# Kernel tuning notes

Measured on AMD Instinct MI355X. Metric: run time of the kernel, lower is better.

## Reference

```python
import jax, jax.numpy as jnp
import numpy as np

EPS = 1e-5
NUM_HEADS = 12
HEAD_DIM = 64


def _split_heads(x, H, hd):
    B, S, _ = x.shape
    return x.reshape(B, S, H, hd).transpose(0, 2, 1, 3)  # [B,H,S,hd]


def _rope_rotate(x, pos, freqs):
    # x: [B,H,S,hd]; pos: [B,S,nd] int; freqs: [nd,H,hd//2]
    ang = jnp.einsum('bsd,dhf->bhsf', pos.astype(x.dtype), freqs)  # [B,H,S,hd//2]
    cos, sin = jnp.cos(ang), jnp.sin(ang)
    B, H, S, hd = x.shape
    xp = x.reshape(B, H, S, hd // 2, 2)
    xr, xi = xp[..., 0], xp[..., 1]
    out = jnp.stack([xr * cos - xi * sin, xr * sin + xi * cos], axis=-1)
    return out.reshape(B, H, S, hd)


def setup_inputs() -> dict:
    key = jax.random.key(0)
    ks = jax.random.split(key, 8)
    B, Sq, Sk, D = 4, 1024, 1024, 768
    return {
        'q': jax.random.normal(ks[0], (B, Sq, D), jnp.float32),
        'kv': jax.random.normal(ks[1], (B, Sk, D), jnp.float32),
        'posq': jax.random.randint(ks[2], (B, Sq, 2), 0, 32, jnp.int32),
        'posk': jax.random.randint(ks[3], (B, Sk, 2), 0, 32, jnp.int32),
        'w_norm': jnp.ones((D,), jnp.float32),
        'w_q': jax.random.normal(ks[4], (D, D), jnp.float32) * 0.02,
        'b_q': jnp.zeros((D,), jnp.float32),
        'w_kv': jax.random.normal(ks[5], (2 * D, D), jnp.float32) * 0.02,
        'b_kv': jnp.zeros((2 * D,), jnp.float32),
        'w_out': jax.random.normal(ks[6], (D, D), jnp.float32) * 0.02,
        'b_out': jnp.zeros((D,), jnp.float32),
        'freqs': jax.random.normal(ks[7], (2, NUM_HEADS, HEAD_DIM // 2), jnp.float32),
    }


def reference(q, kv, posq, posk, w_norm, w_q, b_q, w_kv, b_kv, w_out, b_out, freqs):
    B, Sq, D = q.shape
    H, hd = NUM_HEADS, HEAD_DIM
    # RMSNorm on q
    qn = q * jax.lax.rsqrt(jnp.mean(q * q, axis=-1, keepdims=True) + EPS) * w_norm
    # projections (torch F.linear: x @ W.T + b)
    qp = qn @ w_q.T + b_q
    kvp = kv @ w_kv.T + b_kv
    k, v = jnp.split(kvp, 2, axis=-1)
    qh = _split_heads(qp, H, hd)
    kh = _split_heads(k, H, hd)
    vh = _split_heads(v, H, hd)
    # ND mixed RoPE
    qh = _rope_rotate(qh, posq, freqs)
    kh = _rope_rotate(kh, posk, freqs)
    # SDPA
    scale = 1.0 / np.sqrt(hd)
    scores = jnp.einsum('bhqd,bhkd->bhqk', qh, kh) * scale
    attn = jax.nn.softmax(scores, axis=-1)
    o = jnp.einsum('bhqk,bhkd->bhqd', attn, vh)
    o = o.transpose(0, 2, 1, 3).reshape(B, Sq, H * hd)
    return o @ w_out.T + b_out
```

## Files before the change

kernel.cpp:

```cpp
#include <hip/hip_runtime.h>

#define B_   4
#define S_   1024
#define D_   768
#define H_   12
#define HD_  64
#define NROW (B_*S_)
#define RSTRIDE (H_*HD_)
#define NBH  (B_*H_)
#define LOG2E 1.44269504f

typedef __bf16 bf16_t;
typedef bf16_t bf16x8 __attribute__((ext_vector_type(8)));
typedef float  f32x4  __attribute__((ext_vector_type(4)));
typedef float  f32x16 __attribute__((ext_vector_type(16)));
typedef unsigned int u32x4 __attribute__((ext_vector_type(4)));

__device__ __forceinline__ unsigned short bf16b(float f){
  bf16_t b = (bf16_t)f;
  return __builtin_bit_cast(unsigned short, b);
}

__device__ __forceinline__ void gload16(const void* g, void* l){
  __builtin_amdgcn_global_load_lds(
      (const __attribute__((address_space(1))) void*)g,
      (__attribute__((address_space(3))) void*)l, 16, 0, 0);
}

__device__ __forceinline__ unsigned int cvtpk(float lo, float hi){
  unsigned int r;
  asm("v_cvt_pk_bf16_f32 %0, %1, %2" : "=v"(r) : "v"(lo), "v"(hi));
  return r;
}

__device__ __forceinline__ void plswap(unsigned int &a, unsigned int &b){
  asm volatile("v_permlane32_swap_b32 %0, %1" : "+v"(a), "+v"(b));
}

__global__ void prep_kernel(const float* __restrict__ q, const float* __restrict__ w_norm,
                            bf16_t* __restrict__ qn,
                            const float* __restrict__ wq,  bf16_t* __restrict__ wqb,
                            const float* __restrict__ wkv, bf16_t* __restrict__ wkvb,
                            const float* __restrict__ wo,  bf16_t* __restrict__ wob,
                            const float* __restrict__ kv,  bf16_t* __restrict__ kvb){
  int bid = blockIdx.x;
  if (bid < NROW){
    int row = bid;
    const float* src = q + (size_t)row*D_;
    float vals[3]; float ss = 0.f;
#pragma unroll
    for (int i=0;i<3;i++){ float v = src[threadIdx.x + i*256]; vals[i]=v; ss += v*v; }
#pragma unroll
    for (int m=1;m<64;m<<=1) ss += __shfl_xor(ss, m, 64);
    __shared__ float red[4];
    if ((threadIdx.x & 63) == 0) red[threadIdx.x>>6] = ss;
    __syncthreads();
    float tot = red[0]+red[1]+red[2]+red[3];
    float rs = rsqrtf(tot*(1.0f/D_) + 1e-5f);
#pragma unroll
    for (int i=0;i<3;i++){
      int c = threadIdx.x + i*256;
      qn[(size_t)row*D_ + c] = (bf16_t)(vals[i]*rs*w_norm[c]);
    }
  } else {
    int i = (bid - NROW)*256 + threadIdx.x;
    const int n0 = D_*D_/4, n1 = 2*D_*D_/4, n2 = D_*D_/4, n3 = NROW*D_/4;
    const float* s; bf16_t* d; int off;
    if (i < n0){ s = wq; d = wqb; off = i; }
    else if (i < n0+n1){ s = wkv; d = wkvb; off = i - n0; }
    else if (i < n0+n1+n2){ s = wo; d = wob; off = i - n0 - n1; }
    else if (i < n0+n1+n2+n3){ s = kv; d = kvb; off = i - n0 - n1 - n2; }
    else return;
    float4 v = reinterpret_cast<const float4*>(s)[off];
    ushort4 o;
    o.x = bf16b(v.x); o.y = bf16b(v.y); o.z = bf16b(v.z); o.w = bf16b(v.w);
    reinterpret_cast<ushort4*>(d)[off] = o;
  }
}

template<int TM, int TN>
__device__ __forceinline__ void gemm_core_t(const bf16_t* __restrict__ A, const bf16_t* __restrict__ W,
                                            int K, int row0, int col0,
                                            bf16_t* As, bf16_t* Bs,
                                            f32x4 (&acc)[TM/32][TN/32]){
  const int tid  = threadIdx.x;
  const int lane = tid & 63;
  const int wv   = tid >> 6;
  const int wr = wv >> 1, wc = wv & 1;
  const int l4 = lane >> 4, lm = lane & 15;

  for (int kt = 0; kt < K; kt += 64){
#pragma unroll
    for (int i=0;i<TM/32;i++){
      int c = i*256 + tid;
      int r = c >> 3, kc = (c & 7) ^ (r & 7);
      gload16(A + (size_t)(row0+r)*K + kt + kc*8, As + (size_t)(i*256 + wv*64)*8);
    }
#pragma unroll
    for (int i=0;i<TN/32;i++){
      int c = i*256 + tid;
      int r = c >> 3, kc = (c & 7) ^ (r & 7);
      gload16(W + (size_t)(col0+r)*K + kt + kc*8, Bs + (size_t)(i*256 + wv*64)*8);
    }
    __syncthreads();

#pragma unroll
    for (int kk=0; kk<2; kk++){
      bf16x8 af[TM/32], bfr[TN/32];
#pragma unroll
      for (int mi=0;mi<TM/32;mi++){
        int r = wr*(TM/2) + mi*16 + lm;
        int s = (kk*4 + l4) ^ (r & 7);
        af[mi] = *reinterpret_cast<const bf16x8*>(As + r*64 + s*8);
      }
#pragma unroll
      for (int ni=0;ni<TN/32;ni++){
        int r = wc*(TN/2) + ni*16 + lm;
        int s = (kk*4 + l4) ^ (r & 7);
        bfr[ni] = *reinterpret_cast<const bf16x8*>(Bs + r*64 + s*8);
      }
#pragma unroll
      for (int mi=0;mi<TM/32;mi++)
#pragma unroll
        for (int ni=0;ni<TN/32;ni++)
          acc[mi][ni] = __builtin_amdgcn_mfma_f32_16x16x32_bf16(af[mi], bfr[ni], acc[mi][ni], 0,0,0);
    }
    __syncthreads();
  }
}

__global__ void gemm_kernel(const bf16_t* __restrict__ A, const bf16_t* __restrict__ W,
                            const float* __restrict__ bias, float* __restrict__ C,
                            int N, int K){
  __shared__ bf16_t As[64*64];
  __shared__ bf16_t Bs[64*64];
  int l = ((int)blockIdx.x & 7)*96 + ((int)blockIdx.x >> 3);
  int x = l & 63, y = l >> 6;
  f32x4 acc[2][2] = {};
  gemm_core_t<64,64>(A, W, K, x*64, y*64, As, Bs, acc);
  const int lane = threadIdx.x & 63;
  const int wv   = threadIdx.x >> 6;
  const int wr = wv >> 1, wc = wv & 1;
  const int l4 = lane >> 4, lm = lane & 15;
  const int row0 = x*64, col0 = y*64;
#pragma unroll
  for (int mi=0;mi<2;mi++){
#pragma unroll
    for (int ni=0;ni<2;ni++){
      int col = col0 + wc*32 + ni*16 + lm;
      float bv = bias[col];
#pragma unroll
      for (int j=0;j<4;j++){
        int row = row0 + wr*32 + mi*16 + l4*4 + j;
        C[(size_t)row*N + col] = acc[mi][ni][j] + bv;
      }
    }
  }
}

__device__ __forceinline__ void epi_rope(f32x4 (&acc)[2][4], const float* __restrict__ bias,
                                         const int* __restrict__ pos, const float* __restrict__ freqs,
                                         bf16_t* __restrict__ dst, int row0, int col0, float scale){
  const int lane = threadIdx.x & 63;
  const int wv   = threadIdx.x >> 6;
  const int wr = wv >> 1, wc = wv & 1;
  const int l4 = lane >> 4, lm = lane & 15;
  const int par = lm & 1;
#pragma unroll
  for (int ni=0;ni<4;ni++){
    int col = col0 + wc*64 + ni*16 + lm;
    int h = col >> 6, hd = col & 63, f = hd >> 1;
    float F1 = freqs[h*32 + f];
    float F2 = freqs[H_*32 + h*32 + f];
    float bv = bias[col];
    int cc = f >> 3, hi = (f >> 2) & 1;
    int ebase = cc*512 + hi*256 + (f&3)*2 + par;
#pragma unroll
    for (int mi=0;mi<2;mi++){
#pragma unroll
      for (int j=0;j<4;j++){
        int row = row0 + wr*32 + mi*16 + l4*4 + j;
        float v = acc[mi][ni][j] + bv;
        float vp = __shfl_xor(v, 1, 64);
        float p0 = (float)pos[row*2+0], p1 = (float)pos[row*2+1];
        float ang = p0*F1 + p1*F2;
        float sn, cs;
        __sincosf(ang, &sn, &cs);
        float out = (par ? (vp*sn + v*cs) : (v*cs - vp*sn)) * scale;
        int b = row >> 10, s = row & 1023;
        int bh = b*H_ + h, tile = s >> 5, lq = s & 31;
        dst[((size_t)(bh*32 + tile))*2048 + ebase + lq*8] = (bf16_t)out;
      }
    }
  }
}

__device__ __forceinline__ void epi_vpack(f32x4 (&acc)[2][4], const float* __restrict__ bias,
                                          bf16_t* __restrict__ vfrag, int row0, int col0){
  const int lane = threadIdx.x & 63;
  const int wv   = threadIdx.x >> 6;
  const int wr = wv >> 1, wc = wv & 1;
  const int l4 = lane >> 4, lm = lane & 15;
#pragma unroll
  for (int ni=0;ni<4;ni++){
    int col = col0 + wc*64 + ni*16 + lm;
    int vcol = col - D_;
    int h = vcol >> 6, d = vcol & 63;
    int dt = d >> 5, lq2 = d & 31;
    float bv = bias[col];
    int ebase = dt*1024 + lq2*8;
#pragma unroll
    for (int mi=0;mi<2;mi++){
#pragma unroll
      for (int j=0;j<4;j++){
        int row = row0 + wr*32 + mi*16 + l4*4 + j;
        int b = row >> 10, s = row & 1023;
        int bh = b*H_ + h;
        int kb = s >> 5, ks = (s >> 4) & 1, hi2 = (s >> 3) & 1, jj = s & 7;
        vfrag[((size_t)(bh*32 + kb))*2048 + ebase + ks*512 + hi2*256 + jj]
            = (bf16_t)(acc[mi][ni][j] + bv);
      }
    }
  }
}

__global__ void gemm_qkv_kernel(const bf16_t* __restrict__ qn, const bf16_t* __restrict__ kvb,
                                const bf16_t* __restrict__ wq, const bf16_t* __restrict__ wkv,
                                const float* __restrict__ bq, const float* __restrict__ bkv,
                                const int* __restrict__ posq, const int* __restrict__ posk,
                                const float* __restrict__ freqs,
                                bf16_t* __restrict__ qh, bf16_t* __restrict__ kh,
                                bf16_t* __restrict__ vfrag){
  __shared__ bf16_t As[64*64];
  __shared__ bf16_t Bs[128*64];
  int l = ((int)blockIdx.x & 7)*144 + ((int)blockIdx.x >> 3);
  int x = l & 63, y = l >> 6;
  f32x4 acc[2][4] = {};
  if (y < 6){
    gemm_core_t<64,128>(qn, wq, D_, x*64, y*128, As, Bs, acc);
    epi_rope(acc, bq, posq, freqs, qh, x*64, y*128, 0.125f*LOG2E);
  } else {
    int c0 = (y-6)*128;
    gemm_core_t<64,128>(kvb, wkv, D_, x*64, c0, As, Bs, acc);
    if (y < 12)
      epi_rope(acc, bkv, posk, freqs, kh, x*64, c0, 1.0f);
    else
      epi_vpack(acc, bkv, vfrag, x*64, c0);
  }
}

__device__ __forceinline__ void attn_step(const bf16x8 (&kf)[4], const bf16x8 (&vf)[4],
                                          const bf16x8 (&qf)[4], f32x16 (&acc_o)[2],
                                          float &psum){
  f32x16 accs = {};
#pragma unroll
  for (int c=0;c<4;c++)
    accs = __builtin_amdgcn_mfma_f32_32x32x16_bf16(kf[c], qf[c], accs, 0,0,0);
#pragma unroll
  for (int r=0;r<16;r++){
    float v = exp2f(accs[r]);
    accs[r] = v;
    psum += v;
  }
  bf16x8 pa[2];
#pragma unroll
  for (int ks=0;ks<2;ks++){
    const int base = ks*8;
    unsigned int a0 = cvtpk(accs[base+0], accs[base+1]);
    unsigned int a1 = cvtpk(accs[base+2], accs[base+3]);
    unsigned int b0 = cvtpk(accs[base+4], accs[base+5]);
    unsigned int b1 = cvtpk(accs[base+6], accs[base+7]);
    plswap(a0, b0);
    plswap(a1, b1);
    u32x4 w; w[0]=a0; w[1]=a1; w[2]=b0; w[3]=b1;
    pa[ks] = __builtin_bit_cast(bf16x8, w);
  }
#pragma unroll
  for (int dt=0;dt<2;dt++)
#pragma unroll
    for (int ks=0;ks<2;ks++)
      acc_o[dt] = __builtin_amdgcn_mfma_f32_32x32x16_bf16(pa[ks], vf[dt*2+ks], acc_o[dt], 0,0,0);
}

__global__ __launch_bounds__(256, 3)
void attn_kernel(const bf16_t* __restrict__ Qf, const bf16_t* __restrict__ Kf,
                 const bf16_t* __restrict__ Vf, bf16_t* __restrict__ Oh){
  const int lane = threadIdx.x & 63;
  const int wv   = threadIdx.x >> 6;
  const int hi = lane >> 5, lq = lane & 31;
  int l = ((int)blockIdx.x & 7)*192 + ((int)blockIdx.x >> 3);
  const int bh = l >> 5;
  const int qt = l & 31;
  const int q0 = qt*32;
  const int b = bh / H_, h = bh % H_;
  const size_t headoff = ((size_t)b*S_*H_ + h)*HD_;

  __shared__ float part[4][64][33];
  __shared__ float ps[4][32];

  bf16x8 qf[4];
  {
    const bf16_t* qp_ = Qf + (size_t)(bh*32 + qt)*2048 + lane*8;
#pragma unroll
    for (int c=0;c<4;c++)
      qf[c] = *reinterpret_cast<const bf16x8*>(qp_ + c*512);
  }

  const bf16_t* kbase = Kf + ((size_t)bh*32 + wv*8)*2048 + lane*8;
  const bf16_t* vbase = Vf + ((size_t)bh*32 + wv*8)*2048 + lane*8;

  float psum = 0.f;
  f32x16 acc_o[2] = {};

  bf16x8 kfA[4], kfB[4], vf[4];
#pragma unroll
  for (int c=0;c<4;c++)
    kfA[c] = *reinterpret_cast<const bf16x8*>(kbase + c*512);

#pragma unroll
  for (int t=0; t<4; ++t){
    {
      const bf16_t* vp = vbase + (size_t)(2*t)*2048;
#pragma unroll
      for (int j=0;j<4;j++) vf[j] = *reinterpret_cast<const bf16x8*>(vp + j*512);
      const bf16_t* kp = kbase + (size_t)(2*t+1)*2048;
#pragma unroll
      for (int c=0;c<4;c++) kfB[c] = *reinterpret_cast<const bf16x8*>(kp + c*512);
      attn_step(kfA, vf, qf, acc_o, psum);
    }
    {
      const bf16_t* vp = vbase + (size_t)(2*t+1)*2048;
#pragma unroll
      for (int j=0;j<4;j++) vf[j] = *reinterpret_cast<const bf16x8*>(vp + j*512);
      if (t < 3){
        const bf16_t* kp = kbase + (size_t)(2*t+2)*2048;
#pragma unroll
        for (int c=0;c<4;c++) kfA[c] = *reinterpret_cast<const bf16x8*>(kp + c*512);
      }
      attn_step(kfB, vf, qf, acc_o, psum);
    }
  }

  float tp = psum + __shfl_xor(psum, 32, 64);
#pragma unroll
  for (int dt=0;dt<2;dt++)
#pragma unroll
    for (int r=0;r<16;r++)
      part[wv][lane][dt*16+r] = acc_o[dt][r];
  if (lane < 32) ps[wv][lq] = tp;
  __syncthreads();

  const int dt = wv >> 1;
  const int rbase = (wv & 1)*8;
  float tot = ps[0][lq] + ps[1][lq] + ps[2][lq] + ps[3][lq];
  float inv = 1.0f / tot;

  bf16_t* obase = Oh + headoff;
#pragma unroll
  for (int ri=0;ri<8;ri++){
    int r = rbase + ri;
    float s = part[0][lane][dt*16+r] + part[1][lane][dt*16+r]
            + part[2][lane][dt*16+r] + part[3][lane][dt*16+r];
    float invr = __shfl(inv, (r&3) + 8*(r>>2) + 4*hi, 64);
    int qq = q0 + (r&3) + 8*(r>>2) + 4*hi;
    obase[(size_t)qq*RSTRIDE + dt*32 + lq] = (bf16_t)(s*invr);
  }
}

extern "C" void kernel_launch(void* const* d_in, const int* in_sizes, int n_in,
                              void* d_out, int out_size, void* d_ws, size_t ws_size,
                              hipStream_t stream) {
  const float* q      = (const float*)d_in[0];
  const float* kv     = (const float*)d_in[1];
  const int*   posq   = (const int*)d_in[2];
  const int*   posk   = (const int*)d_in[3];
  const float* w_norm = (const float*)d_in[4];
  const float* w_q    = (const float*)d_in[5];
  const float* b_q    = (const float*)d_in[6];
  const float* w_kv   = (const float*)d_in[7];
  const float* b_kv   = (const float*)d_in[8];
  const float* w_out  = (const float*)d_in[9];
  const float* b_out  = (const float*)d_in[10];
  const float* freqs  = (const float*)d_in[11];
  float* out = (float*)d_out;

  char* p = (char*)d_ws;
  bf16_t* qn   = (bf16_t*)p; p += (size_t)NROW*D_*2;
  bf16_t* kvb  = (bf16_t*)p; p += (size_t)NROW*D_*2;
  bf16_t* wqb  = (bf16_t*)p; p += (size_t)D_*D_*2;
  bf16_t* wkvb = (bf16_t*)p; p += (size_t)2*D_*D_*2;
  bf16_t* wob  = (bf16_t*)p; p += (size_t)D_*D_*2;
  bf16_t* qh   = (bf16_t*)p; p += (size_t)NROW*D_*2;
  bf16_t* kh   = (bf16_t*)p; p += (size_t)NROW*D_*2;
  bf16_t* vt   = (bf16_t*)p; p += (size_t)NBH*HD_*S_*2;
  bf16_t* oh   = (bf16_t*)p; p += (size_t)NROW*D_*2;

  prep_kernel<<<NROW + 5376, 256, 0, stream>>>(q, w_norm, qn,
                                               w_q, wqb, w_kv, wkvb, w_out, wob, kv, kvb);
  gemm_qkv_kernel<<<1152, 256, 0, stream>>>(qn, kvb, wqb, wkvb, b_q, b_kv,
                                            posq, posk, freqs, qh, kh, vt);
  attn_kernel<<<1536, 256, 0, stream>>>(qh, kh, vt, oh);
  gemm_kernel<<<768, 256, 0, stream>>>(oh, wob, b_out, out, D_, D_);
}
```

Baseline: 76.31 us.

## Double-buffer LDS tiles in GEMM cores to overlap loads with MFMA

Splits the GEMM core into separate stage and compute helpers and adds a ping-pong pair of LDS buffers. The next K-tile's global-to-LDS loads are issued before the MFMA work on the current tile, leaving one barrier per iteration instead of two. The goal is to hide global load latency behind matrix compute in both the output projection and the fused QKV+RoPE GEMM. In exchange it doubles LDS use per block, up to 48KB in the QKV kernel, which can lower occupancy.

```diff
diff --git a/kernel.cpp b/kernel.cpp
--- a/kernel.cpp
+++ b/kernel.cpp
@@ -79,65 +79,84 @@
 }
 
 template<int TM, int TN>
-__device__ __forceinline__ void gemm_core_t(const bf16_t* __restrict__ A, const bf16_t* __restrict__ W,
-                                            int K, int row0, int col0,
-                                            bf16_t* As, bf16_t* Bs,
-                                            f32x4 (&acc)[TM/32][TN/32]){
-  const int tid  = threadIdx.x;
-  const int lane = tid & 63;
-  const int wv   = tid >> 6;
+__device__ __forceinline__ void stage_t(const bf16_t* __restrict__ A, const bf16_t* __restrict__ W,
+                                        int K, int row0, int col0, int kt,
+                                        bf16_t* As, bf16_t* Bs){
+  const int tid = threadIdx.x;
+  const int wv  = tid >> 6;
+#pragma unroll
+  for (int i=0;i<TM/32;i++){
+    int c = i*256 + tid;
+    int r = c >> 3, kc = (c & 7) ^ (r & 7);
+    gload16(A + (size_t)(row0+r)*K + kt + kc*8, As + (size_t)(i*256 + wv*64)*8);
+  }
+#pragma unroll
+  for (int i=0;i<TN/32;i++){
+    int c = i*256 + tid;
+    int r = c >> 3, kc = (c & 7) ^ (r & 7);
+    gload16(W + (size_t)(col0+r)*K + kt + kc*8, Bs + (size_t)(i*256 + wv*64)*8);
+  }
+}
+
+template<int TM, int TN>
+__device__ __forceinline__ void compute_t(const bf16_t* As, const bf16_t* Bs,
+                                          f32x4 (&acc)[TM/32][TN/32]){
+  const int lane = threadIdx.x & 63;
+  const int wv   = threadIdx.x >> 6;
   const int wr = wv >> 1, wc = wv & 1;
   const int l4 = lane >> 4, lm = lane & 15;
-
-  for (int kt = 0; kt < K; kt += 64){
-#pragma unroll
-    for (int i=0;i<TM/32;i++){
-      int c = i*256 + tid;
-      int r = c >> 3, kc = (c & 7) ^ (r & 7);
-      gload16(A + (size_t)(row0+r)*K + kt + kc*8, As + (size_t)(i*256 + wv*64)*8);
-    }
-#pragma unroll
-    for (int i=0;i<TN/32;i++){
-      int c = i*256 + tid;
-      int r = c >> 3, kc = (c & 7) ^ (r & 7);
-      gload16(W + (size_t)(col0+r)*K + kt + kc*8, Bs + (size_t)(i*256 + wv*64)*8);
-    }
+#pragma unroll
+  for (int kk=0; kk<2; kk++){
+    bf16x8 af[TM/32], bfr[TN/32];
+#pragma unroll
+    for (int mi=0;mi<TM/32;mi++){
+      int r = wr*(TM/2) + mi*16 + lm;
+      int s = (kk*4 + l4) ^ (r & 7);
+      af[mi] = *reinterpret_cast<const bf16x8*>(As + r*64 + s*8);
+    }
+#pragma unroll
+    for (int ni=0;ni<TN/32;ni++){
+      int r = wc*(TN/2) + ni*16 + lm;
+      int s = (kk*4 + l4) ^ (r & 7);
+      bfr[ni] = *reinterpret_cast<const bf16x8*>(Bs + r*64 + s*8);
+    }
+#pragma unroll
+    for (int mi=0;mi<TM/32;mi++)
+#pragma unroll
+      for (int ni=0;ni<TN/32;ni++)
+        acc[mi][ni] = __builtin_amdgcn_mfma_f32_16x16x32_bf16(af[mi], bfr[ni], acc[mi][ni], 0,0,0);
+  }
+}
+
+template<int TM, int TN>
+__device__ __forceinline__ void gemm_core_db(const bf16_t* __restrict__ A, const bf16_t* __restrict__ W,
+                                             int K, int row0, int col0,
+                                             bf16_t* As0, bf16_t* As1, bf16_t* Bs0, bf16_t* Bs1,
+                                             f32x4 (&acc)[TM/32][TN/32]){
+  stage_t<TM,TN>(A, W, K, row0, col0, 0, As0, Bs0);
+  __syncthreads();
+  const int nt = K/64;
+  bf16_t *Ac = As0, *An = As1, *Bc = Bs0, *Bn = Bs1;
+  for (int t=0; t<nt; ++t){
+    if (t+1 < nt)
+      stage_t<TM,TN>(A, W, K, row0, col0, (t+1)*64, An, Bn);
+    compute_t<TM,TN>(Ac, Bc, acc);
     __syncthreads();
-
-#pragma unroll
-    for (int kk=0; kk<2; kk++){
-      bf16x8 af[TM/32], bfr[TN/32];
-#pragma unroll
-      for (int mi=0;mi<TM/32;mi++){
-        int r = wr*(TM/2) + mi*16 + lm;
-        int s = (kk*4 + l4) ^ (r & 7);
-        af[mi] = *reinterpret_cast<const bf16x8*>(As + r*64 + s*8);
-      }
-#pragma unroll
-      for (int ni=0;ni<TN/32;ni++){
-        int r = wc*(TN/2) + ni*16 + lm;
-        int s = (kk*4 + l4) ^ (r & 7);
-        bfr[ni] = *reinterpret_cast<const bf16x8*>(Bs + r*64 + s*8);
-      }
-#pragma unroll
-      for (int mi=0;mi<TM/32;mi++)
-#pragma unroll
-        for (int ni=0;ni<TN/32;ni++)
-          acc[mi][ni] = __builtin_amdgcn_mfma_f32_16x16x32_bf16(af[mi], bfr[ni], acc[mi][ni], 0,0,0);
-    }
-    __syncthreads();
+    bf16_t* tmp;
+    tmp = Ac; Ac = An; An = tmp;
+    tmp = Bc; Bc = Bn; Bn = tmp;
   }
 }
 
 __global__ void gemm_kernel(const bf16_t* __restrict__ A, const bf16_t* __restrict__ W,
                             const float* __restrict__ bias, float* __restrict__ C,
                             int N, int K){
-  __shared__ bf16_t As[64*64];
-  __shared__ bf16_t Bs[64*64];
+  __shared__ bf16_t As[2][64*64];
+  __shared__ bf16_t Bs[2][64*64];
   int l = ((int)blockIdx.x & 7)*96 + ((int)blockIdx.x >> 3);
   int x = l & 63, y = l >> 6;
   f32x4 acc[2][2] = {};
-  gemm_core_t<64,64>(A, W, K, x*64, y*64, As, Bs, acc);
+  gemm_core_db<64,64>(A, W, K, x*64, y*64, As[0], As[1], Bs[0], Bs[1], acc);
   const int lane = threadIdx.x & 63;
   const int wv   = threadIdx.x >> 6;
   const int wr = wv >> 1, wc = wv & 1;
@@ -231,17 +250,17 @@
                                 const float* __restrict__ freqs,
                                 bf16_t* __restrict__ qh, bf16_t* __restrict__ kh,
                                 bf16_t* __restrict__ vfrag){
-  __shared__ bf16_t As[64*64];
-  __shared__ bf16_t Bs[128*64];
+  __shared__ bf16_t As[2][64*64];
+  __shared__ bf16_t Bs[2][128*64];
   int l = ((int)blockIdx.x & 7)*144 + ((int)blockIdx.x >> 3);
   int x = l & 63, y = l >> 6;
   f32x4 acc[2][4] = {};
   if (y < 6){
-    gemm_core_t<64,128>(qn, wq, D_, x*64, y*128, As, Bs, acc);
+    gemm_core_db<64,128>(qn, wq, D_, x*64, y*128, As[0], As[1], Bs[0], Bs[1], acc);
     epi_rope(acc, bq, posq, freqs, qh, x*64, y*128, 0.125f*LOG2E);
   } else {
     int c0 = (y-6)*128;
-    gemm_core_t<64,128>(kvb, wkv, D_, x*64, c0, As, Bs, acc);
+    gemm_core_db<64,128>(kvb, wkv, D_, x*64, c0, As[0], As[1], Bs[0], Bs[1], acc);
     if (y < 12)
       epi_rope(acc, bkv, posk, freqs, kh, x*64, c0, 1.0f);
     else
```

Result: no change. 74.90 us, median of 2 (-1.9%).
